# Performance work log

Hardware: AMD Instinct MI355X
Metric: run time of the kernel (lower is better)

The kernel has to match this reference:

```python
import jax, jax.numpy as jnp
import numpy as np

B, T, D, U = 32, 2048, 512, 512

def setup_inputs() -> dict:
    key = jax.random.key(0)
    ks = jax.random.split(key, 8)
    s = 0.02
    return {
        "query": jax.random.normal(ks[0], (B, D), dtype=jnp.float32),
        "values": jax.random.normal(ks[1], (B, T, D), dtype=jnp.float32),
        "W1_w": jax.random.normal(ks[2], (D, U), dtype=jnp.float32) * s,
        "W1_b": jnp.zeros((U,), dtype=jnp.float32),
        "W2_w": jax.random.normal(ks[3], (D, U), dtype=jnp.float32) * s,
        "W2_b": jnp.zeros((U,), dtype=jnp.float32),
        "V_w": jax.random.normal(ks[4], (U, 1), dtype=jnp.float32) * s,
        "V_b": jnp.zeros((1,), dtype=jnp.float32),
    }

def reference(query, values, W1_w, W1_b, W2_w, W2_b, V_w, V_b):
    # query: [B, D] -> [B, 1, U]; values: [B, T, D] -> [B, T, U]
    q_proj = (query @ W1_w + W1_b)[:, None, :]              # [B, 1, U]
    v_proj = jnp.einsum('btd,du->btu', values, W2_w) + W2_b  # [B, T, U]
    score = jnp.tanh(q_proj + v_proj) @ V_w + V_b            # [B, T, 1]
    attn = jax.nn.softmax(score, axis=1)                     # [B, T, 1]
    context = jnp.sum(attn * values, axis=1)                 # [B, D]
    return context, attn
```

## Files before the change

### kernel.cpp

```cpp
#include <hip/hip_runtime.h>
#include <hip/hip_bf16.h>
#include <cstddef>

#define B_ 32
#define T_ 2048
#define D_ 512
#define U_ 512

typedef __attribute__((ext_vector_type(8))) short bf16x8;
typedef __attribute__((ext_vector_type(4))) float f32x4;

__device__ __forceinline__ unsigned short f2bf(float f) {
  union { float f; unsigned u; } x; x.f = f;
  unsigned r = x.u + 0x7fffu + ((x.u >> 16) & 1u);
  return (unsigned short)(r >> 16);
}
__device__ __forceinline__ unsigned pack2bf(float a, float b) {
  return (unsigned)f2bf(a) | ((unsigned)f2bf(b) << 16);
}
__device__ __forceinline__ float tanh_fast(float x) {
  float e = __expf(2.0f * x);
  return 1.0f - 2.0f * __builtin_amdgcn_rcpf(e + 1.0f);
}

__global__ void k0_pack(const float* __restrict__ W2, unsigned* __restrict__ W2P) {
  const int tid = threadIdx.x;
  #pragma unroll
  for (int ii = 0; ii < 2; ++ii) {
    int p = blockIdx.x * 512 + ii * 256 + tid;
    int j = (p & 3) * 2;
    int l = (p >> 2) & 63;
    int t = p >> 8;
    int u = (t >> 4) * 16 + (l & 15);
    int k = (t & 15) * 32 + ((l >> 4) << 3) + j;
    float f0 = W2[(size_t)k * U_ + u];
    float f1 = W2[(size_t)(k + 1) * U_ + u];
    W2P[p] = pack2bf(f0, f1);
  }
}

__global__ void k1_qp(const float* __restrict__ query, const float* __restrict__ W1,
                      const float* __restrict__ W1b, const float* __restrict__ W2b,
                      float* __restrict__ qp, float* __restrict__ score,
                      float* __restrict__ ctx) {
  __shared__ float qs[D_];
  const int blk = blockIdx.x;
  const int b = blk >> 1, uh = (blk & 1) * 256;
  const int tid = threadIdx.x;
  qs[tid] = query[b * D_ + tid];
  qs[tid + 256] = query[b * D_ + tid + 256];
  __syncthreads();
  const int u = uh + tid;
  float a0 = 0, a1 = 0, a2 = 0, a3 = 0, a4 = 0, a5 = 0, a6 = 0, a7 = 0;
  for (int d = 0; d < D_; d += 8) {
    a0 += qs[d + 0] * W1[(size_t)(d + 0) * U_ + u];
    a1 += qs[d + 1] * W1[(size_t)(d + 1) * U_ + u];
    a2 += qs[d + 2] * W1[(size_t)(d + 2) * U_ + u];
    a3 += qs[d + 3] * W1[(size_t)(d + 3) * U_ + u];
    a4 += qs[d + 4] * W1[(size_t)(d + 4) * U_ + u];
    a5 += qs[d + 5] * W1[(size_t)(d + 5) * U_ + u];
    a6 += qs[d + 6] * W1[(size_t)(d + 6) * U_ + u];
    a7 += qs[d + 7] * W1[(size_t)(d + 7) * U_ + u];
  }
  qp[b * U_ + u] = ((a0 + a1) + (a2 + a3)) + ((a4 + a5) + (a6 + a7)) + W1b[u] + W2b[u];
  const int gt = blk * 256 + tid;
  ctx[gt] = 0.0f;
  #pragma unroll
  for (int i = 0; i < 4; ++i) score[i * 16384 + gt] = 0.0f;
}

__global__ __launch_bounds__(256, 2) void k2_score(
    const float* __restrict__ values, const unsigned short* __restrict__ W2P,
    const float* __restrict__ qp, const float* __restrict__ Vw,
    float* __restrict__ score) {
  constexpr int LS = 264;
  __shared__ unsigned short av[64 * LS];
  __shared__ float qv[U_];
  __shared__ float vwv[U_];
  const int tid = threadIdx.x;
  const int m0 = blockIdx.x * 64;
  const int b = m0 >> 11;
  qv[tid] = qp[b * U_ + tid];        qv[tid + 256] = qp[b * U_ + tid + 256];
  vwv[tid] = Vw[tid];                vwv[tid + 256] = Vw[tid + 256];

  const int l = tid & 63, w = tid >> 6;
  const int lr = l & 15, lq = l >> 4;

  f32x4 acc[4][8];
  #pragma unroll
  for (int mi = 0; mi < 4; ++mi)
    #pragma unroll
    for (int ni = 0; ni < 8; ++ni) acc[mi][ni] = (f32x4){0.f, 0.f, 0.f, 0.f};

  const unsigned short* bw = W2P + (size_t)(w * 8) * 8192 + (size_t)l * 8;
  const int abase = lr * LS + lq * 8;

  #pragma unroll
  for (int half = 0; half < 2; ++half) {
    const float4* vb = (const float4*)(values + (size_t)m0 * D_ + half * 256);
    #pragma unroll
    for (int it = 0; it < 16; ++it) {
      int i = tid + it * 256;
      int row = i >> 6, c4 = i & 63;
      float4 v = vb[(size_t)row * 128 + c4];
      uint2 p; p.x = pack2bf(v.x, v.y); p.y = pack2bf(v.z, v.w);
      *(uint2*)&av[row * LS + c4 * 4] = p;
    }
    __syncthreads();
    const int kg0 = half * 8;
    bf16x8 b0[8], b1[8];
    #pragma unroll
    for (int ni = 0; ni < 8; ++ni)
      b0[ni] = *(const bf16x8*)(bw + (size_t)ni * 8192 + (size_t)kg0 * 512);
    #pragma unroll
    for (int kk = 0; kk < 8; ++kk) {
      bf16x8* cur = (kk & 1) ? b1 : b0;
      bf16x8* nxt = (kk & 1) ? b0 : b1;
      if (kk < 7) {
        #pragma unroll
        for (int ni = 0; ni < 8; ++ni)
          nxt[ni] = *(const bf16x8*)(bw + (size_t)ni * 8192 + (size_t)(kg0 + kk + 1) * 512);
      }
      bf16x8 a[4];
      #pragma unroll
      for (int mi = 0; mi < 4; ++mi)
        a[mi] = *(const bf16x8*)&av[abase + mi * 16 * LS + kk * 32];
      #pragma unroll
      for (int ni = 0; ni < 8; ++ni)
        #pragma unroll
        for (int mi = 0; mi < 4; ++mi)
          acc[mi][ni] = __builtin_amdgcn_mfma_f32_16x16x32_bf16(a[mi], cur[ni], acc[mi][ni], 0, 0, 0);
    }
    __syncthreads();
  }

  float sacc[4][4];
  #pragma unroll
  for (int mi = 0; mi < 4; ++mi)
    #pragma unroll
    for (int r = 0; r < 4; ++r) sacc[mi][r] = 0.0f;
  #pragma unroll
  for (int ni = 0; ni < 8; ++ni) {
    int u = w * 128 + ni * 16 + lr;
    float qpv = qv[u], vv = vwv[u];
    #pragma unroll
    for (int mi = 0; mi < 4; ++mi)
      #pragma unroll
      for (int r = 0; r < 4; ++r)
        sacc[mi][r] += tanh_fast(acc[mi][ni][r] + qpv) * vv;
  }
  #pragma unroll
  for (int mi = 0; mi < 4; ++mi)
    #pragma unroll
    for (int r = 0; r < 4; ++r) {
      float v = sacc[mi][r];
      v += __shfl_xor(v, 1); v += __shfl_xor(v, 2);
      v += __shfl_xor(v, 4); v += __shfl_xor(v, 8);
      if (lr == 0) atomicAdd(&score[m0 + mi * 16 + lq * 4 + r], v);
    }
}

__global__ void k3_softmax(const float* __restrict__ score, float* __restrict__ attn) {
  __shared__ float red[8];
  const int b = blockIdx.x, tid = threadIdx.x;
  const float* s = score + b * T_;
  float v[8];
  float mx = -1e30f;
  #pragma unroll
  for (int i = 0; i < 8; ++i) { v[i] = s[tid + i * 256]; mx = fmaxf(mx, v[i]); }
  #pragma unroll
  for (int off = 1; off < 64; off <<= 1) mx = fmaxf(mx, __shfl_xor(mx, off));
  if ((tid & 63) == 0) red[tid >> 6] = mx;
  __syncthreads();
  mx = fmaxf(fmaxf(red[0], red[1]), fmaxf(red[2], red[3]));
  float sum = 0.0f;
  #pragma unroll
  for (int i = 0; i < 8; ++i) { v[i] = __expf(v[i] - mx); sum += v[i]; }
  #pragma unroll
  for (int off = 1; off < 64; off <<= 1) sum += __shfl_xor(sum, off);
  if ((tid & 63) == 0) red[4 + (tid >> 6)] = sum;
  __syncthreads();
  sum = (red[4] + red[5]) + (red[6] + red[7]);
  float inv = 1.0f / sum;
  #pragma unroll
  for (int i = 0; i < 8; ++i) attn[b * T_ + tid + i * 256] = v[i] * inv;
}

__global__ void k4_ctx(const float* __restrict__ values, const float* __restrict__ attn,
                       float* __restrict__ ctx) {
  __shared__ float at[64];
  __shared__ float ps[512];
  const int blk = blockIdx.x;
  const int b = blk >> 5, tc = blk & 31;
  const int tid = threadIdx.x;
  if (tid < 64) at[tid] = attn[b * T_ + tc * 64 + tid];
  __syncthreads();
  const int q = tid & 127;
  const int r0 = tid >> 7;
  const float4* vb = (const float4*)(values + ((size_t)b * T_ + tc * 64) * D_);
  float ax = 0.f, ay = 0.f, az = 0.f, aw = 0.f;
  #pragma unroll 8
  for (int tt = 0; tt < 32; ++tt) {
    int row = tt * 2 + r0;
    float4 v = vb[(size_t)row * 128 + q];
    float a = at[row];
    ax += a * v.x; ay += a * v.y; az += a * v.z; aw += a * v.w;
  }
  if (r0 == 1) { ps[4 * q] = ax; ps[4 * q + 1] = ay; ps[4 * q + 2] = az; ps[4 * q + 3] = aw; }
  __syncthreads();
  if (r0 == 0) {
    atomicAdd(&ctx[b * D_ + 4 * q + 0], ax + ps[4 * q + 0]);
    atomicAdd(&ctx[b * D_ + 4 * q + 1], ay + ps[4 * q + 1]);
    atomicAdd(&ctx[b * D_ + 4 * q + 2], az + ps[4 * q + 2]);
    atomicAdd(&ctx[b * D_ + 4 * q + 3], aw + ps[4 * q + 3]);
  }
}

extern "C" void kernel_launch(void* const* d_in, const int* in_sizes, int n_in,
                              void* d_out, int out_size, void* d_ws, size_t ws_size,
                              hipStream_t stream) {
  const float* query = (const float*)d_in[0];
  const float* values = (const float*)d_in[1];
  const float* W1w = (const float*)d_in[2];
  const float* W1b = (const float*)d_in[3];
  const float* W2w = (const float*)d_in[4];
  const float* W2b = (const float*)d_in[5];
  const float* Vw  = (const float*)d_in[6];

  float* out = (float*)d_out;
  float* ctx  = out;
  float* attn = out + B_ * D_;
  float* score = attn;

  char* ws = (char*)d_ws;
  unsigned* W2P = (unsigned*)ws;
  float* qp    = (float*)(ws + 512 * 1024);

  k0_pack<<<256, 256, 0, stream>>>(W2w, W2P);
  k1_qp<<<64, 256, 0, stream>>>(query, W1w, W1b, W2b, qp, score, ctx);
  k2_score<<<1024, 256, 0, stream>>>(values, (const unsigned short*)W2P, qp, Vw, score);
  k3_softmax<<<32, 256, 0, stream>>>(score, attn);
  k4_ctx<<<1024, 256, 0, stream>>>(values, attn, ctx);
}
```

Baseline: 298.3 us.

## Split score GEMM across U halves and merge prep kernels into one launch

The W2 packing kernel and the query-projection/zeroing kernel are merged into a single launch that branches on block index, saving one launch. The score kernel now splits the U dimension across two blocks per 64-row tile, doubling the grid to 2048 blocks. This halves the accumulator and B-fragment registers and raises the occupancy hint from 2 to 3 blocks per CU. The cost is that each 64-row values tile is loaded from HBM and converted to bf16 twice, and there are twice as many atomic adds into score.

```diff
diff --git a/kernel.cpp b/kernel.cpp
--- a/kernel.cpp
+++ b/kernel.cpp
@@ -23,76 +23,77 @@
   return 1.0f - 2.0f * __builtin_amdgcn_rcpf(e + 1.0f);
 }
 
-__global__ void k0_pack(const float* __restrict__ W2, unsigned* __restrict__ W2P) {
+__global__ void kA_prep(const float* __restrict__ W2, unsigned* __restrict__ W2P,
+                        const float* __restrict__ query, const float* __restrict__ W1,
+                        const float* __restrict__ W1b, const float* __restrict__ W2b,
+                        float* __restrict__ qp, float* __restrict__ score,
+                        float* __restrict__ ctx) {
   const int tid = threadIdx.x;
-  #pragma unroll
-  for (int ii = 0; ii < 2; ++ii) {
-    int p = blockIdx.x * 512 + ii * 256 + tid;
-    int j = (p & 3) * 2;
-    int l = (p >> 2) & 63;
-    int t = p >> 8;
-    int u = (t >> 4) * 16 + (l & 15);
-    int k = (t & 15) * 32 + ((l >> 4) << 3) + j;
-    float f0 = W2[(size_t)k * U_ + u];
-    float f1 = W2[(size_t)(k + 1) * U_ + u];
-    W2P[p] = pack2bf(f0, f1);
-  }
-}
-
-__global__ void k1_qp(const float* __restrict__ query, const float* __restrict__ W1,
-                      const float* __restrict__ W1b, const float* __restrict__ W2b,
-                      float* __restrict__ qp, float* __restrict__ score,
-                      float* __restrict__ ctx) {
-  __shared__ float qs[D_];
-  const int blk = blockIdx.x;
-  const int b = blk >> 1, uh = (blk & 1) * 256;
-  const int tid = threadIdx.x;
-  qs[tid] = query[b * D_ + tid];
-  qs[tid + 256] = query[b * D_ + tid + 256];
-  __syncthreads();
-  const int u = uh + tid;
-  float a0 = 0, a1 = 0, a2 = 0, a3 = 0, a4 = 0, a5 = 0, a6 = 0, a7 = 0;
-  for (int d = 0; d < D_; d += 8) {
-    a0 += qs[d + 0] * W1[(size_t)(d + 0) * U_ + u];
-    a1 += qs[d + 1] * W1[(size_t)(d + 1) * U_ + u];
-    a2 += qs[d + 2] * W1[(size_t)(d + 2) * U_ + u];
-    a3 += qs[d + 3] * W1[(size_t)(d + 3) * U_ + u];
-    a4 += qs[d + 4] * W1[(size_t)(d + 4) * U_ + u];
-    a5 += qs[d + 5] * W1[(size_t)(d + 5) * U_ + u];
-    a6 += qs[d + 6] * W1[(size_t)(d + 6) * U_ + u];
-    a7 += qs[d + 7] * W1[(size_t)(d + 7) * U_ + u];
-  }
-  qp[b * U_ + u] = ((a0 + a1) + (a2 + a3)) + ((a4 + a5) + (a6 + a7)) + W1b[u] + W2b[u];
-  const int gt = blk * 256 + tid;
-  ctx[gt] = 0.0f;
-  #pragma unroll
-  for (int i = 0; i < 4; ++i) score[i * 16384 + gt] = 0.0f;
-}
-
-__global__ __launch_bounds__(256, 2) void k2_score(
+  if (blockIdx.x < 256) {
+    #pragma unroll
+    for (int ii = 0; ii < 2; ++ii) {
+      int p = blockIdx.x * 512 + ii * 256 + tid;
+      int j = (p & 3) * 2;
+      int l = (p >> 2) & 63;
+      int t = p >> 8;
+      int u = (t >> 4) * 16 + (l & 15);
+      int k = (t & 15) * 32 + ((l >> 4) << 3) + j;
+      W2P[p] = pack2bf(W2[(size_t)k * U_ + u], W2[(size_t)(k + 1) * U_ + u]);
+    }
+  } else {
+    __shared__ float qs[D_];
+    const int blk = blockIdx.x - 256;
+    const int b = blk >> 1, uhh = (blk & 1) * 256;
+    qs[tid] = query[b * D_ + tid];
+    qs[tid + 256] = query[b * D_ + tid + 256];
+    __syncthreads();
+    const int u = uhh + tid;
+    float a0 = 0, a1 = 0, a2 = 0, a3 = 0, a4 = 0, a5 = 0, a6 = 0, a7 = 0;
+    for (int d = 0; d < D_; d += 8) {
+      a0 += qs[d + 0] * W1[(size_t)(d + 0) * U_ + u];
+      a1 += qs[d + 1] * W1[(size_t)(d + 1) * U_ + u];
+      a2 += qs[d + 2] * W1[(size_t)(d + 2) * U_ + u];
+      a3 += qs[d + 3] * W1[(size_t)(d + 3) * U_ + u];
+      a4 += qs[d + 4] * W1[(size_t)(d + 4) * U_ + u];
+      a5 += qs[d + 5] * W1[(size_t)(d + 5) * U_ + u];
+      a6 += qs[d + 6] * W1[(size_t)(d + 6) * U_ + u];
+      a7 += qs[d + 7] * W1[(size_t)(d + 7) * U_ + u];
+    }
+    qp[b * U_ + u] = ((a0 + a1) + (a2 + a3)) + ((a4 + a5) + (a6 + a7)) + W1b[u] + W2b[u];
+    const int gt = blk * 256 + tid;
+    ctx[gt] = 0.0f;
+    #pragma unroll
+    for (int i = 0; i < 4; ++i) score[i * 16384 + gt] = 0.0f;
+  }
+}
+
+__global__ __launch_bounds__(256, 3) void k2_score(
     const float* __restrict__ values, const unsigned short* __restrict__ W2P,
     const float* __restrict__ qp, const float* __restrict__ Vw,
     float* __restrict__ score) {
   constexpr int LS = 264;
   __shared__ unsigned short av[64 * LS];
-  __shared__ float qv[U_];
-  __shared__ float vwv[U_];
+  __shared__ float qv[256];
+  __shared__ float vwv[256];
   const int tid = threadIdx.x;
-  const int m0 = blockIdx.x * 64;
+  const int bx = blockIdx.x;
+  const int mt = bx >> 1, uh = bx & 1;
+  const int m0 = mt * 64;
   const int b = m0 >> 11;
-  qv[tid] = qp[b * U_ + tid];        qv[tid + 256] = qp[b * U_ + tid + 256];
-  vwv[tid] = Vw[tid];                vwv[tid + 256] = Vw[tid + 256];
+  const int ub = uh * 256;
+  qv[tid] = qp[b * U_ + ub + tid];
+  vwv[tid] = Vw[ub + tid];
 
   const int l = tid & 63, w = tid >> 6;
   const int lr = l & 15, lq = l >> 4;
 
-  f32x4 acc[4][8];
+  f32x4 acc[4][4];
   #pragma unroll
   for (int mi = 0; mi < 4; ++mi)
     #pragma unroll
-    for (int ni = 0; ni < 8; ++ni) acc[mi][ni] = (f32x4){0.f, 0.f, 0.f, 0.f};
-
-  const unsigned short* bw = W2P + (size_t)(w * 8) * 8192 + (size_t)l * 8;
+    for (int ni = 0; ni < 4; ++ni) acc[mi][ni] = (f32x4){0.f, 0.f, 0.f, 0.f};
+
+  const unsigned short* bw = W2P + (size_t)(uh * 16 + w * 4) * 8192 + (size_t)l * 8;
   const int abase = lr * LS + lq * 8;
 
   #pragma unroll
@@ -108,9 +109,9 @@
     }
     __syncthreads();
     const int kg0 = half * 8;
-    bf16x8 b0[8], b1[8];
-    #pragma unroll
-    for (int ni = 0; ni < 8; ++ni)
+    bf16x8 b0[4], b1[4];
+    #pragma unroll
+    for (int ni = 0; ni < 4; ++ni)
       b0[ni] = *(const bf16x8*)(bw + (size_t)ni * 8192 + (size_t)kg0 * 512);
     #pragma unroll
     for (int kk = 0; kk < 8; ++kk) {
@@ -118,7 +119,7 @@
       bf16x8* nxt = (kk & 1) ? b0 : b1;
       if (kk < 7) {
         #pragma unroll
-        for (int ni = 0; ni < 8; ++ni)
+        for (int ni = 0; ni < 4; ++ni)
           nxt[ni] = *(const bf16x8*)(bw + (size_t)ni * 8192 + (size_t)(kg0 + kk + 1) * 512);
       }
       bf16x8 a[4];
@@ -126,7 +127,7 @@
       for (int mi = 0; mi < 4; ++mi)
         a[mi] = *(const bf16x8*)&av[abase + mi * 16 * LS + kk * 32];
       #pragma unroll
-      for (int ni = 0; ni < 8; ++ni)
+      for (int ni = 0; ni < 4; ++ni)
         #pragma unroll
         for (int mi = 0; mi < 4; ++mi)
           acc[mi][ni] = __builtin_amdgcn_mfma_f32_16x16x32_bf16(a[mi], cur[ni], acc[mi][ni], 0, 0, 0);
@@ -140,9 +141,9 @@
     #pragma unroll
     for (int r = 0; r < 4; ++r) sacc[mi][r] = 0.0f;
   #pragma unroll
-  for (int ni = 0; ni < 8; ++ni) {
-    int u = w * 128 + ni * 16 + lr;
-    float qpv = qv[u], vv = vwv[u];
+  for (int ni = 0; ni < 4; ++ni) {
+    int ul = w * 64 + ni * 16 + lr;
+    float qpv = qv[ul], vv = vwv[ul];
     #pragma unroll
     for (int mi = 0; mi < 4; ++mi)
       #pragma unroll
@@ -236,9 +237,8 @@
   unsigned* W2P = (unsigned*)ws;
   float* qp    = (float*)(ws + 512 * 1024);
 
-  k0_pack<<<256, 256, 0, stream>>>(W2w, W2P);
-  k1_qp<<<64, 256, 0, stream>>>(query, W1w, W1b, W2b, qp, score, ctx);
-  k2_score<<<1024, 256, 0, stream>>>(values, (const unsigned short*)W2P, qp, Vw, score);
+  kA_prep<<<320, 256, 0, stream>>>(W2w, W2P, query, W1w, W1b, W2b, qp, score, ctx);
+  k2_score<<<2048, 256, 0, stream>>>(values, (const unsigned short*)W2P, qp, Vw, score);
   k3_softmax<<<32, 256, 0, stream>>>(score, attn);
   k4_ctx<<<1024, 256, 0, stream>>>(values, attn, ctx);
 }
```

Measured after the change: 296.8 us. About the same (-0.5%).
